# Performance work log

Hardware: AMD Instinct MI355X
Metric: run time of the kernel (lower is better)

Reference implementation:

```python
import jax, jax.numpy as jnp
import numpy as np

DEC_H = 1024
ENC_H_TOTAL = 1024  # enc_hid_size * enc_num_dirs


def setup_inputs() -> dict:
    key = jax.random.key(0)
    ks = jax.random.split(key, 10)
    N, L = 64, 1024
    s = 0.02
    return {
        "dec_h_curr": jax.random.normal(ks[0], (N, DEC_H), jnp.float32),
        "enc_hids": jax.random.normal(ks[1], (N, L, ENC_H_TOTAL), jnp.float32),
        # project_dec_hids: Linear(dec_H, dec_H)
        "W_dec": jax.random.normal(ks[2], (DEC_H, DEC_H), jnp.float32) * s,
        "b_dec": jnp.zeros((DEC_H,), jnp.float32),
        # project_enc_hids: Linear(enc_H*nDir, dec_H)
        "W_enc": jax.random.normal(ks[3], (ENC_H_TOTAL, DEC_H), jnp.float32) * s,
        "b_enc": jnp.zeros((DEC_H,), jnp.float32),
        # project_to_one_dim: Linear(dec_H, 1)
        "W_one": jax.random.normal(ks[4], (DEC_H, 1), jnp.float32) * s,
        "b_one": jnp.zeros((1,), jnp.float32),
        # project_att_hids: Linear(enc_H*nDir, dec_H)
        "W_att": jax.random.normal(ks[5], (ENC_H_TOTAL, DEC_H), jnp.float32) * s,
        "b_att": jnp.zeros((DEC_H,), jnp.float32),
    }


def reference(dec_h_curr, enc_hids, W_dec, b_dec, W_enc, b_enc, W_one, b_one, W_att, b_att):
    # additive (Bahdanau) attention branch
    d = dec_h_curr @ W_dec + b_dec                     # N x dec_H
    e = jnp.einsum('nle,ed->nld', enc_hids, W_enc) + b_enc  # N x L x dec_H
    scores = jnp.einsum('nld,do->nl', jnp.tanh(d[:, None, :] + e), W_one) + b_one[0]  # N x L
    alpha = jax.nn.softmax(scores, axis=-1)            # N x L
    ctx = jnp.einsum('nl,nle->ne', alpha, enc_hids)    # N x enc_H_total
    h_att_curr = ctx @ W_att + b_att                   # N x dec_H
    return h_att_curr, alpha
```

## Files before the change

### kernel.cpp

```cpp
#include <hip/hip_runtime.h>
#include <cstdio>
#include <cstdint>


typedef __bf16 bf16x8 __attribute__((ext_vector_type(8)));
typedef float f32x4 __attribute__((ext_vector_type(4)));
typedef unsigned short us8 __attribute__((ext_vector_type(8)));

static __device__ __forceinline__ unsigned short f2b(float f) {
  union { float f; unsigned u; } v; v.f = f;
  unsigned r = (v.u + 0x7fffu + ((v.u >> 16) & 1u)) >> 16;
  return (unsigned short)r;
}
static __device__ __forceinline__ float b2f(unsigned short u) {
  union { unsigned u; float f; } v; v.u = ((unsigned)u) << 16;
  return v.f;
}
static __device__ __forceinline__ void gl_lds16(const void* g, void* l) {
  __builtin_amdgcn_global_load_lds(
      (const __attribute__((address_space(1))) unsigned int*)g,
      (__attribute__((address_space(3))) unsigned int*)l, 16, 0, 0);
}
static __device__ __forceinline__ float fast_tanh(float x) {
  float ax = __builtin_fminf(__builtin_fabsf(x), 18.0f);
  float u = __builtin_amdgcn_exp2f(ax * 2.88539008177792681f);
  float t = (u - 1.0f) * __builtin_amdgcn_rcpf(u + 1.0f);
  return __builtin_copysignf(t, x);
}

__global__ __launch_bounds__(256) void prep_k(
    const float* __restrict__ enc, unsigned short* __restrict__ Ap,
    const float* __restrict__ W_enc, unsigned short* __restrict__ Bp,
    const float* __restrict__ dec_h, const float* __restrict__ W_dec,
    const float* __restrict__ b_dec, const float* __restrict__ b_enc,
    float* __restrict__ addterm) {
  __shared__ __align__(16) unsigned short tile[8192];
  const int bid = blockIdx.x;
  const int t = threadIdx.x;

  if (bid < 128) {
    const int Tn = bid >> 4, kt = bid & 15;
    #pragma unroll
    for (int it = 0; it < 8; ++it) {
      int idx = it * 256 + t;
      int kk = idx >> 5, n4 = idx & 31;
      const float4 v = *(const float4*)(W_enc + (size_t)(kt * 64 + kk) * 1024 + Tn * 128 + n4 * 4);
      int c = kk >> 3, j = kk & 7;
      #pragma unroll
      for (int x = 0; x < 4; ++x) {
        int mm = n4 * 4 + x;
        float fv = (x == 0) ? v.x : (x == 1) ? v.y : (x == 2) ? v.z : v.w;
        tile[(mm * 8 + (c ^ (mm & 7))) * 8 + j] = f2b(fv);
      }
    }
    __syncthreads();
    #pragma unroll
    for (int it = 0; it < 4; ++it) {
      int p = it * 256 + t;
      int c = p >> 7, m = p & 127;
      us8 v = *(const us8*)&tile[(m * 8 + (c ^ (m & 7))) * 8];
      *(us8*)(Bp + ((size_t)bid * 1024 + p) * 8) = v;
    }
  } else if (bid < 384) {
    const int bid2 = bid - 128;
    const int jb = bid2 & 3, n = bid2 >> 2;
    float* xs = (float*)tile;
    for (int i = t; i < 1024; i += 256) xs[i] = dec_h[n * 1024 + i];
    __syncthreads();
    int j = jb * 256 + t;
    float s = 0.f;
    #pragma unroll 8
    for (int k = 0; k < 1024; ++k) s += xs[k] * W_dec[(size_t)k * 1024 + j];
    addterm[n * 1024 + j] = s + b_dec[j] + b_enc[j];
  } else {
    const int ba = bid - 384;
    const int T = ba >> 4, kt = ba & 15;
    #pragma unroll
    for (int it = 0; it < 8; ++it) {
      int idx = it * 256 + t;
      int m = idx >> 4, c4 = idx & 15;
      const float4 v = *(const float4*)(enc + (size_t)(T * 128 + m) * 1024 + kt * 64 + c4 * 4);
      ushort4 o;
      o.x = f2b(v.x); o.y = f2b(v.y); o.z = f2b(v.z); o.w = f2b(v.w);
      int c = c4 >> 1, half = c4 & 1;
      *(ushort4*)&tile[(m * 8 + (c ^ (m & 7))) * 8 + half * 4] = o;
    }
    __syncthreads();
    #pragma unroll
    for (int it = 0; it < 4; ++it) {
      int p = it * 256 + t;
      int c = p >> 7, m = p & 127;
      us8 v = *(const us8*)&tile[(m * 8 + (c ^ (m & 7))) * 8];
      *(us8*)(Ap + ((size_t)ba * 1024 + p) * 8) = v;
    }
  }
}

__global__ __launch_bounds__(512, 2) void score_gemm(
    const unsigned short* __restrict__ Ap, const unsigned short* __restrict__ Bp,
    const float* __restrict__ addterm, const float* __restrict__ Wone,
    float* __restrict__ spart) {
  __shared__ __align__(16) unsigned short lA[32768];
  __shared__ __align__(16) unsigned short lB[32768];
  const int tid = threadIdx.x;
  const int lane = tid & 63, wave = tid >> 6;
  const int wm = wave >> 2, wn = wave & 3;
  const int q = lane >> 4, r = lane & 15;

  const int flat = blockIdx.x;
  const int tl = (flat & 7) * 128 + (flat >> 3);
  const int nb = tl & 3, mb = tl >> 2;

  f32x4 acc[8][4];
  #pragma unroll
  for (int i = 0; i < 8; ++i)
    #pragma unroll
    for (int j = 0; j < 4; ++j) acc[i][j] = (f32x4){0.f, 0.f, 0.f, 0.f};

  const unsigned short* pA0 = Ap + (((size_t)(2 * mb + 0) * 16384) + tid) * 8;
  const unsigned short* pA1 = Ap + (((size_t)(2 * mb + 1) * 16384) + tid) * 8;
  const unsigned short* pB0 = Bp + (((size_t)(2 * nb + 0) * 16384) + tid) * 8;
  const unsigned short* pB1 = Bp + (((size_t)(2 * nb + 1) * 16384) + tid) * 8;

  const unsigned short* rdA = &lA[(wm * 512 + q * 128 + r) * 8];
  const unsigned short* rdB = &lB[((wn >> 1) * 512 + q * 128 + (wn & 1) * 64 + r) * 8];

  bf16x8 af[4], bg[4];

#define SA(h, off, u) gl_lds16(((h) ? pA1 : pA0) + (size_t)(off) * 4096, \
                               &lA[(((u) * 1024 + (h) * 512 + wave * 64) * 8)])
#define SB(h, off, u) gl_lds16(((h) ? pB1 : pB0) + (size_t)(off) * 4096, \
                               &lB[(((u) * 1024 + (h) * 512 + wave * 64) * 8)])
#define RD_BG(u) { \
  bg[0] = *(const bf16x8*)&rdB[((u) * 1024 +  0) * 8]; \
  bg[1] = *(const bf16x8*)&rdB[((u) * 1024 + 16) * 8]; \
  bg[2] = *(const bf16x8*)&rdB[((u) * 1024 + 32) * 8]; \
  bg[3] = *(const bf16x8*)&rdB[((u) * 1024 + 48) * 8]; }
#define RD_AF(u, mh) { \
  af[0] = *(const bf16x8*)&rdA[((u) * 1024 + (mh) * 64 +  0) * 8]; \
  af[1] = *(const bf16x8*)&rdA[((u) * 1024 + (mh) * 64 + 16) * 8]; \
  af[2] = *(const bf16x8*)&rdA[((u) * 1024 + (mh) * 64 + 32) * 8]; \
  af[3] = *(const bf16x8*)&rdA[((u) * 1024 + (mh) * 64 + 48) * 8]; }
#define MMA_CORE(mh) \
  __builtin_amdgcn_s_barrier(); \
  asm volatile("s_waitcnt lgkmcnt(0)" ::: "memory"); \
  __builtin_amdgcn_sched_barrier(0); \
  __builtin_amdgcn_s_setprio(1); \
  acc[(mh)*4+0][0] = __builtin_amdgcn_mfma_f32_16x16x32_bf16(af[0], bg[0], acc[(mh)*4+0][0], 0, 0, 0); \
  acc[(mh)*4+0][1] = __builtin_amdgcn_mfma_f32_16x16x32_bf16(af[0], bg[1], acc[(mh)*4+0][1], 0, 0, 0); \
  acc[(mh)*4+0][2] = __builtin_amdgcn_mfma_f32_16x16x32_bf16(af[0], bg[2], acc[(mh)*4+0][2], 0, 0, 0); \
  acc[(mh)*4+0][3] = __builtin_amdgcn_mfma_f32_16x16x32_bf16(af[0], bg[3], acc[(mh)*4+0][3], 0, 0, 0); \
  acc[(mh)*4+1][0] = __builtin_amdgcn_mfma_f32_16x16x32_bf16(af[1], bg[0], acc[(mh)*4+1][0], 0, 0, 0); \
  acc[(mh)*4+1][1] = __builtin_amdgcn_mfma_f32_16x16x32_bf16(af[1], bg[1], acc[(mh)*4+1][1], 0, 0, 0); \
  acc[(mh)*4+1][2] = __builtin_amdgcn_mfma_f32_16x16x32_bf16(af[1], bg[2], acc[(mh)*4+1][2], 0, 0, 0); \
  acc[(mh)*4+1][3] = __builtin_amdgcn_mfma_f32_16x16x32_bf16(af[1], bg[3], acc[(mh)*4+1][3], 0, 0, 0); \
  acc[(mh)*4+2][0] = __builtin_amdgcn_mfma_f32_16x16x32_bf16(af[2], bg[0], acc[(mh)*4+2][0], 0, 0, 0); \
  acc[(mh)*4+2][1] = __builtin_amdgcn_mfma_f32_16x16x32_bf16(af[2], bg[1], acc[(mh)*4+2][1], 0, 0, 0); \
  acc[(mh)*4+2][2] = __builtin_amdgcn_mfma_f32_16x16x32_bf16(af[2], bg[2], acc[(mh)*4+2][2], 0, 0, 0); \
  acc[(mh)*4+2][3] = __builtin_amdgcn_mfma_f32_16x16x32_bf16(af[2], bg[3], acc[(mh)*4+2][3], 0, 0, 0); \
  acc[(mh)*4+3][0] = __builtin_amdgcn_mfma_f32_16x16x32_bf16(af[3], bg[0], acc[(mh)*4+3][0], 0, 0, 0); \
  acc[(mh)*4+3][1] = __builtin_amdgcn_mfma_f32_16x16x32_bf16(af[3], bg[1], acc[(mh)*4+3][1], 0, 0, 0); \
  acc[(mh)*4+3][2] = __builtin_amdgcn_mfma_f32_16x16x32_bf16(af[3], bg[2], acc[(mh)*4+3][2], 0, 0, 0); \
  acc[(mh)*4+3][3] = __builtin_amdgcn_mfma_f32_16x16x32_bf16(af[3], bg[3], acc[(mh)*4+3][3], 0, 0, 0); \
  __builtin_amdgcn_s_setprio(0);
#define BAR __builtin_amdgcn_s_barrier()
#define VM8 asm volatile("s_waitcnt vmcnt(8)" ::: "memory")
#define VM4 asm volatile("s_waitcnt vmcnt(4)" ::: "memory")
#define VM0 asm volatile("s_waitcnt vmcnt(0)" ::: "memory")

  SA(0, 0, 0); SA(1, 0, 0); SB(0, 0, 0); SB(1, 0, 0);
  SA(0, 1, 1); SA(1, 1, 1); SB(0, 1, 1); SB(1, 1, 1);
  SA(0, 2, 2); SA(1, 2, 2); SB(0, 2, 2); SB(1, 2, 2);
  VM8;
  BAR;

  #pragma unroll 1
  for (int it2 = 0; it2 < 7; ++it2) {
    RD_BG(0); RD_AF(0, 0); SA(0, 3, 3); SA(1, 3, 3); MMA_CORE(0); BAR;
    RD_AF(0, 1);           SB(0, 3, 3); SB(1, 3, 3); MMA_CORE(1); VM8; BAR;
    RD_BG(1); RD_AF(1, 0); SA(0, 4, 0); SA(1, 4, 0); MMA_CORE(0); BAR;
    RD_AF(1, 1);           SB(0, 4, 0); SB(1, 4, 0); MMA_CORE(1); VM8; BAR;
    RD_BG(2); RD_AF(2, 0); SA(0, 5, 1); SA(1, 5, 1); MMA_CORE(0); BAR;
    RD_AF(2, 1);           SB(0, 5, 1); SB(1, 5, 1); MMA_CORE(1); VM8; BAR;
    RD_BG(3); RD_AF(3, 0); SA(0, 6, 2); SA(1, 6, 2); MMA_CORE(0); BAR;
    RD_AF(3, 1);           SB(0, 6, 2); SB(1, 6, 2); MMA_CORE(1); VM8; BAR;
    pA0 += 4 * 4096; pA1 += 4 * 4096; pB0 += 4 * 4096; pB1 += 4 * 4096;
  }

  RD_BG(0); RD_AF(0, 0); SA(0, 3, 3); SA(1, 3, 3); MMA_CORE(0); BAR;
  RD_AF(0, 1);           SB(0, 3, 3); SB(1, 3, 3); MMA_CORE(1); VM8; BAR;
  RD_BG(1); RD_AF(1, 0); MMA_CORE(0); BAR;
  RD_AF(1, 1);           MMA_CORE(1); VM4; BAR;
  RD_BG(2); RD_AF(2, 0); MMA_CORE(0); BAR;
  RD_AF(2, 1);           MMA_CORE(1); VM0; BAR;
  RD_BG(3); RD_AF(3, 0); MMA_CORE(0); BAR;
  RD_AF(3, 1);           MMA_CORE(1);

#undef SA
#undef SB
#undef RD_BG
#undef RD_AF
#undef MMA_CORE
#undef BAR
#undef VM8
#undef VM4
#undef VM0

  const int nrow = mb >> 2;
  float addv[4], wv[4];
  #pragma unroll
  for (int ni = 0; ni < 4; ++ni) {
    int col = nb * 256 + wn * 64 + ni * 16 + r;
    addv[ni] = addterm[nrow * 1024 + col];
    wv[ni] = Wone[col];
  }
  #pragma unroll
  for (int mi = 0; mi < 8; ++mi) {
    #pragma unroll
    for (int rr = 0; rr < 4; ++rr) {
      float s = 0.f;
      #pragma unroll
      for (int ni = 0; ni < 4; ++ni)
        s += fast_tanh(acc[mi][ni][rr] + addv[ni]) * wv[ni];
      s += __shfl_xor(s, 1);
      s += __shfl_xor(s, 2);
      s += __shfl_xor(s, 4);
      s += __shfl_xor(s, 8);
      if (r == 0) {
        size_t row = (size_t)mb * 256 + wm * 128 + mi * 16 + q * 4 + rr;
        spart[row * 16 + nb * 4 + wn] = s;
      }
    }
  }
}

__global__ __launch_bounds__(256) void ctx_fused(
    const float* __restrict__ spart, float* __restrict__ alpha,
    const unsigned short* __restrict__ Ap, float* __restrict__ ctx) {
  const int kt = blockIdx.x, n = blockIdx.y, t = threadIdx.x;
  __shared__ float red[8];
  __shared__ float al[1024];

  float sv[4];
  #pragma unroll
  for (int i = 0; i < 4; ++i) {
    int l = i * 256 + t;
    const float4* p = (const float4*)(spart + ((size_t)n * 1024 + l) * 16);
    float4 v0 = p[0], v1 = p[1], v2 = p[2], v3 = p[3];
    sv[i] = (v0.x + v0.y + v0.z + v0.w) + (v1.x + v1.y + v1.z + v1.w) +
            (v2.x + v2.y + v2.z + v2.w) + (v3.x + v3.y + v3.z + v3.w);
  }
  float m = fmaxf(fmaxf(sv[0], sv[1]), fmaxf(sv[2], sv[3]));
  for (int o = 32; o > 0; o >>= 1) m = fmaxf(m, __shfl_xor(m, o));
  if ((t & 63) == 0) red[t >> 6] = m;
  __syncthreads();
  float gm = fmaxf(fmaxf(red[0], red[1]), fmaxf(red[2], red[3]));
  float e[4], s = 0.f;
  #pragma unroll
  for (int i = 0; i < 4; ++i) { e[i] = expf(sv[i] - gm); s += e[i]; }
  for (int o = 32; o > 0; o >>= 1) s += __shfl_xor(s, o);
  if ((t & 63) == 0) red[4 + (t >> 6)] = s;
  __syncthreads();
  float inv = 1.0f / (red[4] + red[5] + red[6] + red[7]);
  #pragma unroll
  for (int i = 0; i < 4; ++i) {
    float a = e[i] * inv;
    al[i * 256 + t] = a;
    if (kt == 0) alpha[(size_t)n * 1024 + i * 256 + t] = a;
  }
  __syncthreads();

  const int c = t >> 5, ls = t & 31;
  float acc[8] = {0.f, 0.f, 0.f, 0.f, 0.f, 0.f, 0.f, 0.f};
  #pragma unroll 4
  for (int lb = 0; lb < 32; ++lb) {
    int l = lb * 32 + ls;
    int M = n * 1024 + l;
    int T = M >> 7, mm = M & 127;
    us8 v = *(const us8*)(Ap + ((((size_t)T * 16 + kt) * 8 + c) * 128 + mm) * 8);
    float w = al[l];
    #pragma unroll
    for (int j = 0; j < 8; ++j) acc[j] += w * b2f(v[j]);
  }
  #pragma unroll
  for (int off = 1; off <= 16; off <<= 1)
    #pragma unroll
    for (int j = 0; j < 8; ++j) acc[j] += __shfl_xor(acc[j], off);
  if (ls == 0) {
    #pragma unroll
    for (int j = 0; j < 8; ++j) ctx[(size_t)n * 1024 + kt * 64 + c * 8 + j] = acc[j];
  }
}

__global__ __launch_bounds__(256) void hatt_k(
    const float* __restrict__ ctx, const float* __restrict__ W_att,
    const float* __restrict__ b_att, float* __restrict__ out) {
  __shared__ float cs[1024];
  __shared__ float red[4][64];
  const int n = blockIdx.y;
  const int jb = blockIdx.x;
  const int t = threadIdx.x;
  for (int i = t; i < 1024; i += 256) cs[i] = ctx[(size_t)n * 1024 + i];
  __syncthreads();
  const int j = jb * 64 + (t & 63);
  const int ks = t >> 6;
  float s = 0.f;
  const float* Wp = W_att + (size_t)(ks * 256) * 1024 + j;
  #pragma unroll 8
  for (int k = 0; k < 256; ++k) s += cs[ks * 256 + k] * Wp[(size_t)k * 1024];
  red[ks][t & 63] = s;
  __syncthreads();
  if (t < 64) {
    out[(size_t)n * 1024 + jb * 64 + t] =
        red[0][t] + red[1][t] + red[2][t] + red[3][t] + b_att[jb * 64 + t];
  }
}

extern "C" void kernel_launch(void* const* d_in, const int* in_sizes, int n_in,
                              void* d_out, int out_size, void* d_ws, size_t ws_size,
                              hipStream_t stream) {
  const float* dec_h = (const float*)d_in[0];
  const float* enc   = (const float*)d_in[1];
  const float* W_dec = (const float*)d_in[2];
  const float* b_dec = (const float*)d_in[3];
  const float* W_enc = (const float*)d_in[4];
  const float* b_enc = (const float*)d_in[5];
  const float* W_one = (const float*)d_in[6];
  const float* W_att = (const float*)d_in[8];
  const float* b_att = (const float*)d_in[9];
  float* out = (float*)d_out;

  char* ws = (char*)d_ws;
  const size_t OFF_A   = 0;
  const size_t OFF_B   = 134217728;
  const size_t OFF_ADD = OFF_B + 2097152;
  const size_t OFF_SP  = OFF_ADD + 262144;
  const size_t OFF_CTX = OFF_SP + 4194304;
  const size_t NEED    = OFF_CTX + 262144;
  if (ws_size < NEED) {
    fprintf(stderr, "kernel_launch: ws too small (%zu < %zu)\n", ws_size, NEED);
    return;
  }
  unsigned short* Ap = (unsigned short*)(ws + OFF_A);
  unsigned short* Bp = (unsigned short*)(ws + OFF_B);
  float* addterm = (float*)(ws + OFF_ADD);
  float* spart   = (float*)(ws + OFF_SP);
  float* ctx     = (float*)(ws + OFF_CTX);
  float* alpha   = out + 65536;

  prep_k<<<8576, 256, 0, stream>>>(enc, Ap, W_enc, Bp, dec_h, W_dec, b_dec, b_enc, addterm);
  score_gemm<<<1024, 512, 0, stream>>>(Ap, Bp, addterm, W_one, spart);
  ctx_fused<<<dim3(16, 64), 256, 0, stream>>>(spart, alpha, Ap, ctx);
  hatt_k<<<dim3(16, 64), 256, 0, stream>>>(ctx, W_att, b_att, out);
}
```

Baseline: 631.7 us.

## Restructure score GEMM main loop to one barrier per K-step; split dterm kernel

The score GEMM inner loop now loads all eight A fragments and four B fragments per K-step, issues all four async global->LDS loads at once, and runs 32 MFMAs between a single wait/barrier pair. This halves the number of barriers and waitcnt stalls per K-step, reducing synchronisation overhead, at the cost of more VGPRs for fragments. The decoder projection (dec_h @ W_dec) is moved out of the prep kernel into its own small kernel, which adds one launch but removes the mixed-role blocks from prep_k.

```diff
diff --git a/kernel.cpp b/kernel.cpp
--- a/kernel.cpp
+++ b/kernel.cpp
@@ -30,10 +30,7 @@
 
 __global__ __launch_bounds__(256) void prep_k(
     const float* __restrict__ enc, unsigned short* __restrict__ Ap,
-    const float* __restrict__ W_enc, unsigned short* __restrict__ Bp,
-    const float* __restrict__ dec_h, const float* __restrict__ W_dec,
-    const float* __restrict__ b_dec, const float* __restrict__ b_enc,
-    float* __restrict__ addterm) {
+    const float* __restrict__ W_enc, unsigned short* __restrict__ Bp) {
   __shared__ __align__(16) unsigned short tile[8192];
   const int bid = blockIdx.x;
   const int t = threadIdx.x;
@@ -61,19 +58,8 @@
       us8 v = *(const us8*)&tile[(m * 8 + (c ^ (m & 7))) * 8];
       *(us8*)(Bp + ((size_t)bid * 1024 + p) * 8) = v;
     }
-  } else if (bid < 384) {
-    const int bid2 = bid - 128;
-    const int jb = bid2 & 3, n = bid2 >> 2;
-    float* xs = (float*)tile;
-    for (int i = t; i < 1024; i += 256) xs[i] = dec_h[n * 1024 + i];
-    __syncthreads();
-    int j = jb * 256 + t;
-    float s = 0.f;
-    #pragma unroll 8
-    for (int k = 0; k < 1024; ++k) s += xs[k] * W_dec[(size_t)k * 1024 + j];
-    addterm[n * 1024 + j] = s + b_dec[j] + b_enc[j];
   } else {
-    const int ba = bid - 384;
+    const int ba = bid - 128;
     const int T = ba >> 4, kt = ba & 15;
     #pragma unroll
     for (int it = 0; it < 8; ++it) {
@@ -94,6 +80,23 @@
       *(us8*)(Ap + ((size_t)ba * 1024 + p) * 8) = v;
     }
   }
+}
+
+__global__ __launch_bounds__(256) void dterm_k(
+    const float* __restrict__ dec_h, const float* __restrict__ W_dec,
+    const float* __restrict__ b_dec, const float* __restrict__ b_enc,
+    float* __restrict__ addterm) {
+  __shared__ float xs[1024];
+  const int bid2 = blockIdx.x;
+  const int jb = bid2 & 3, n = bid2 >> 2;
+  const int t = threadIdx.x;
+  for (int i = t; i < 1024; i += 256) xs[i] = dec_h[n * 1024 + i];
+  __syncthreads();
+  int j = jb * 256 + t;
+  float s = 0.f;
+  #pragma unroll 8
+  for (int k = 0; k < 1024; ++k) s += xs[k] * W_dec[(size_t)k * 1024 + j];
+  addterm[n * 1024 + j] = s + b_dec[j] + b_enc[j];
 }
 
 __global__ __launch_bounds__(512, 2) void score_gemm(
@@ -125,43 +128,35 @@
   const unsigned short* rdA = &lA[(wm * 512 + q * 128 + r) * 8];
   const unsigned short* rdB = &lB[((wn >> 1) * 512 + q * 128 + (wn & 1) * 64 + r) * 8];
 
-  bf16x8 af[4], bg[4];
+  bf16x8 af[8], bg[4];
 
 #define SA(h, off, u) gl_lds16(((h) ? pA1 : pA0) + (size_t)(off) * 4096, \
                                &lA[(((u) * 1024 + (h) * 512 + wave * 64) * 8)])
 #define SB(h, off, u) gl_lds16(((h) ? pB1 : pB0) + (size_t)(off) * 4096, \
                                &lB[(((u) * 1024 + (h) * 512 + wave * 64) * 8)])
-#define RD_BG(u) { \
+#define RDS(u) { \
   bg[0] = *(const bf16x8*)&rdB[((u) * 1024 +  0) * 8]; \
   bg[1] = *(const bf16x8*)&rdB[((u) * 1024 + 16) * 8]; \
   bg[2] = *(const bf16x8*)&rdB[((u) * 1024 + 32) * 8]; \
-  bg[3] = *(const bf16x8*)&rdB[((u) * 1024 + 48) * 8]; }
-#define RD_AF(u, mh) { \
-  af[0] = *(const bf16x8*)&rdA[((u) * 1024 + (mh) * 64 +  0) * 8]; \
-  af[1] = *(const bf16x8*)&rdA[((u) * 1024 + (mh) * 64 + 16) * 8]; \
-  af[2] = *(const bf16x8*)&rdA[((u) * 1024 + (mh) * 64 + 32) * 8]; \
-  af[3] = *(const bf16x8*)&rdA[((u) * 1024 + (mh) * 64 + 48) * 8]; }
-#define MMA_CORE(mh) \
-  __builtin_amdgcn_s_barrier(); \
+  bg[3] = *(const bf16x8*)&rdB[((u) * 1024 + 48) * 8]; \
+  af[0] = *(const bf16x8*)&rdA[((u) * 1024 +   0) * 8]; \
+  af[1] = *(const bf16x8*)&rdA[((u) * 1024 +  16) * 8]; \
+  af[2] = *(const bf16x8*)&rdA[((u) * 1024 +  32) * 8]; \
+  af[3] = *(const bf16x8*)&rdA[((u) * 1024 +  48) * 8]; \
+  af[4] = *(const bf16x8*)&rdA[((u) * 1024 +  64) * 8]; \
+  af[5] = *(const bf16x8*)&rdA[((u) * 1024 +  80) * 8]; \
+  af[6] = *(const bf16x8*)&rdA[((u) * 1024 +  96) * 8]; \
+  af[7] = *(const bf16x8*)&rdA[((u) * 1024 + 112) * 8]; }
+#define MMA32 \
   asm volatile("s_waitcnt lgkmcnt(0)" ::: "memory"); \
   __builtin_amdgcn_sched_barrier(0); \
   __builtin_amdgcn_s_setprio(1); \
-  acc[(mh)*4+0][0] = __builtin_amdgcn_mfma_f32_16x16x32_bf16(af[0], bg[0], acc[(mh)*4+0][0], 0, 0, 0); \
-  acc[(mh)*4+0][1] = __builtin_amdgcn_mfma_f32_16x16x32_bf16(af[0], bg[1], acc[(mh)*4+0][1], 0, 0, 0); \
-  acc[(mh)*4+0][2] = __builtin_amdgcn_mfma_f32_16x16x32_bf16(af[0], bg[2], acc[(mh)*4+0][2], 0, 0, 0); \
-  acc[(mh)*4+0][3] = __builtin_amdgcn_mfma_f32_16x16x32_bf16(af[0], bg[3], acc[(mh)*4+0][3], 0, 0, 0); \
-  acc[(mh)*4+1][0] = __builtin_amdgcn_mfma_f32_16x16x32_bf16(af[1], bg[0], acc[(mh)*4+1][0], 0, 0, 0); \
-  acc[(mh)*4+1][1] = __builtin_amdgcn_mfma_f32_16x16x32_bf16(af[1], bg[1], acc[(mh)*4+1][1], 0, 0, 0); \
-  acc[(mh)*4+1][2] = __builtin_amdgcn_mfma_f32_16x16x32_bf16(af[1], bg[2], acc[(mh)*4+1][2], 0, 0, 0); \
-  acc[(mh)*4+1][3] = __builtin_amdgcn_mfma_f32_16x16x32_bf16(af[1], bg[3], acc[(mh)*4+1][3], 0, 0, 0); \
-  acc[(mh)*4+2][0] = __builtin_amdgcn_mfma_f32_16x16x32_bf16(af[2], bg[0], acc[(mh)*4+2][0], 0, 0, 0); \
-  acc[(mh)*4+2][1] = __builtin_amdgcn_mfma_f32_16x16x32_bf16(af[2], bg[1], acc[(mh)*4+2][1], 0, 0, 0); \
-  acc[(mh)*4+2][2] = __builtin_amdgcn_mfma_f32_16x16x32_bf16(af[2], bg[2], acc[(mh)*4+2][2], 0, 0, 0); \
-  acc[(mh)*4+2][3] = __builtin_amdgcn_mfma_f32_16x16x32_bf16(af[2], bg[3], acc[(mh)*4+2][3], 0, 0, 0); \
-  acc[(mh)*4+3][0] = __builtin_amdgcn_mfma_f32_16x16x32_bf16(af[3], bg[0], acc[(mh)*4+3][0], 0, 0, 0); \
-  acc[(mh)*4+3][1] = __builtin_amdgcn_mfma_f32_16x16x32_bf16(af[3], bg[1], acc[(mh)*4+3][1], 0, 0, 0); \
-  acc[(mh)*4+3][2] = __builtin_amdgcn_mfma_f32_16x16x32_bf16(af[3], bg[2], acc[(mh)*4+3][2], 0, 0, 0); \
-  acc[(mh)*4+3][3] = __builtin_amdgcn_mfma_f32_16x16x32_bf16(af[3], bg[3], acc[(mh)*4+3][3], 0, 0, 0); \
+  _Pragma("unroll") \
+  for (int mi_ = 0; mi_ < 8; ++mi_) { \
+    _Pragma("unroll") \
+    for (int ni_ = 0; ni_ < 4; ++ni_) \
+      acc[mi_][ni_] = __builtin_amdgcn_mfma_f32_16x16x32_bf16(af[mi_], bg[ni_], acc[mi_][ni_], 0, 0, 0); \
+  } \
   __builtin_amdgcn_s_setprio(0);
 #define BAR __builtin_amdgcn_s_barrier()
 #define VM8 asm volatile("s_waitcnt vmcnt(8)" ::: "memory")
@@ -176,31 +171,22 @@
 
   #pragma unroll 1
   for (int it2 = 0; it2 < 7; ++it2) {
-    RD_BG(0); RD_AF(0, 0); SA(0, 3, 3); SA(1, 3, 3); MMA_CORE(0); BAR;
-    RD_AF(0, 1);           SB(0, 3, 3); SB(1, 3, 3); MMA_CORE(1); VM8; BAR;
-    RD_BG(1); RD_AF(1, 0); SA(0, 4, 0); SA(1, 4, 0); MMA_CORE(0); BAR;
-    RD_AF(1, 1);           SB(0, 4, 0); SB(1, 4, 0); MMA_CORE(1); VM8; BAR;
-    RD_BG(2); RD_AF(2, 0); SA(0, 5, 1); SA(1, 5, 1); MMA_CORE(0); BAR;
-    RD_AF(2, 1);           SB(0, 5, 1); SB(1, 5, 1); MMA_CORE(1); VM8; BAR;
-    RD_BG(3); RD_AF(3, 0); SA(0, 6, 2); SA(1, 6, 2); MMA_CORE(0); BAR;
-    RD_AF(3, 1);           SB(0, 6, 2); SB(1, 6, 2); MMA_CORE(1); VM8; BAR;
+    RDS(0); SA(0, 3, 3); SA(1, 3, 3); SB(0, 3, 3); SB(1, 3, 3); MMA32; VM8; BAR;
+    RDS(1); SA(0, 4, 0); SA(1, 4, 0); SB(0, 4, 0); SB(1, 4, 0); MMA32; VM8; BAR;
+    RDS(2); SA(0, 5, 1); SA(1, 5, 1); SB(0, 5, 1); SB(1, 5, 1); MMA32; VM8; BAR;
+    RDS(3); SA(0, 6, 2); SA(1, 6, 2); SB(0, 6, 2); SB(1, 6, 2); MMA32; VM8; BAR;
     pA0 += 4 * 4096; pA1 += 4 * 4096; pB0 += 4 * 4096; pB1 += 4 * 4096;
   }
 
-  RD_BG(0); RD_AF(0, 0); SA(0, 3, 3); SA(1, 3, 3); MMA_CORE(0); BAR;
-  RD_AF(0, 1);           SB(0, 3, 3); SB(1, 3, 3); MMA_CORE(1); VM8; BAR;
-  RD_BG(1); RD_AF(1, 0); MMA_CORE(0); BAR;
-  RD_AF(1, 1);           MMA_CORE(1); VM4; BAR;
-  RD_BG(2); RD_AF(2, 0); MMA_CORE(0); BAR;
-  RD_AF(2, 1);           MMA_CORE(1); VM0; BAR;
-  RD_BG(3); RD_AF(3, 0); MMA_CORE(0); BAR;
-  RD_AF(3, 1);           MMA_CORE(1);
+  RDS(0); SA(0, 3, 3); SA(1, 3, 3); SB(0, 3, 3); SB(1, 3, 3); MMA32; VM8; BAR;
+  RDS(1); MMA32; VM4; BAR;
+  RDS(2); MMA32; VM0; BAR;
+  RDS(3); MMA32;
 
 #undef SA
 #undef SB
-#undef RD_BG
-#undef RD_AF
-#undef MMA_CORE
+#undef RDS
+#undef MMA32
 #undef BAR
 #undef VM8
 #undef VM4
@@ -348,7 +334,8 @@
   float* ctx     = (float*)(ws + OFF_CTX);
   float* alpha   = out + 65536;
 
-  prep_k<<<8576, 256, 0, stream>>>(enc, Ap, W_enc, Bp, dec_h, W_dec, b_dec, b_enc, addterm);
+  prep_k<<<8320, 256, 0, stream>>>(enc, Ap, W_enc, Bp);
+  dterm_k<<<256, 256, 0, stream>>>(dec_h, W_dec, b_dec, b_enc, addterm);
   score_gemm<<<1024, 512, 0, stream>>>(Ap, Bp, addterm, W_one, spart);
   ctx_fused<<<dim3(16, 64), 256, 0, stream>>>(spart, alpha, Ap, ctx);
   hatt_k<<<dim3(16, 64), 256, 0, stream>>>(ctx, W_att, b_att, out);
```

After: 650.8 us. 1.03x slower.
